# Optimization experiments

Measured on AMD Instinct MI355X. Metric: run time of the kernel, lower is better.

Reference implementation:

```python
import jax, jax.numpy as jnp
import numpy as np

C = 64
CQ = C // 4
G = 8  # group norm groups
EPS_GN = 1e-5
POS_COEF = 0.1


def setup_inputs() -> dict:
    key = jax.random.key(0)
    ks = jax.random.split(key, 12)
    B, N = 2, 4096
    return {
        "context_features": jax.random.normal(ks[0], (B, C, N), jnp.float32),
        "motion_features": jax.random.normal(ks[1], (B, C, N), jnp.float32),
        "xyz1": jax.random.uniform(ks[2], (B, N, 3), jnp.float32),
        # tied q/k conv weight (Conv1d k=1, no bias): (C//4, C)
        "Wqk": jax.random.normal(ks[3], (CQ, C), jnp.float32) * 0.1,
        # v_conv: Conv1d(C, C, 1) with bias
        "Wv": jax.random.normal(ks[4], (C, C), jnp.float32) * 0.1,
        "bv": jax.random.normal(ks[5], (C,), jnp.float32) * 0.1,
        # trans_conv: Conv1d(C, C, 1) with bias
        "Wt": jax.random.normal(ks[6], (C, C), jnp.float32) * 0.1,
        "bt": jax.random.normal(ks[7], (C,), jnp.float32) * 0.1,
        # GroupNorm(8, C) affine params
        "gn_w": jax.random.normal(ks[8], (C,), jnp.float32) * 0.1 + 1.0,
        "gn_b": jax.random.normal(ks[9], (C,), jnp.float32) * 0.1,
        # PReLU single slope, alpha_gma scalar (init 0 in torch; random here for testing)
        "prelu_a": jnp.float32(0.25) + jax.random.normal(ks[10], (), jnp.float32) * 0.01,
        "alpha": jax.random.normal(ks[11], (), jnp.float32) * 0.1,
    }


def _group_norm(x, w, b):
    # x: (B, C, N)
    B, Cc, N = x.shape
    xg = x.reshape(B, G, Cc // G, N)
    mu = xg.mean(axis=(2, 3), keepdims=True)
    var = xg.var(axis=(2, 3), keepdims=True)
    xn = ((xg - mu) * jax.lax.rsqrt(var + EPS_GN)).reshape(B, Cc, N)
    return xn * w[None, :, None] + b[None, :, None]


def reference(context_features, motion_features, xyz1, Wqk, Wv, bv, Wt, bt, gn_w, gn_b, prelu_a, alpha):
    # --- self attention (tied q/k) ---
    q = jnp.einsum("oc,bcn->bon", Wqk, context_features)  # (B, C/4, N)
    corr = jnp.einsum("bom,bon->bmn", q, q)               # (B, N, N)
    attn = jax.nn.softmax(corr, axis=-1)
    attn = attn / (1e-9 + attn.sum(axis=1, keepdims=True))

    # --- position mask via Gram-trick squared distances ---
    sq = jnp.sum(xyz1 * xyz1, axis=-1)                    # (B, N)
    d = sq[:, :, None] + sq[:, None, :] - 2.0 * jnp.einsum("bid,bjd->bij", xyz1, xyz1)
    d = jnp.maximum(d, 0.0)
    pos_am = d / (1e-9 + d.sum(axis=1, keepdims=True))
    mask = pos_am <= POS_COEF

    local = attn * mask
    local = jax.nn.softmax(local, axis=-1)
    local = local / (1e-9 + local.sum(axis=1, keepdims=True))
    attn = attn + local

    # --- GMA fusion ---
    xv = jnp.einsum("oc,bcn->bon", Wv, motion_features) + bv[None, :, None]
    gma = jnp.einsum("bcm,bmn->bcn", xv, attn)
    res = jnp.einsum("oc,bcn->bon", Wt, motion_features - gma) + bt[None, :, None]
    gr = _group_norm(res, gn_w, gn_b)
    gr = jnp.where(gr >= 0, gr, prelu_a * gr)  # PReLU
    return alpha * gr + motion_features
```

## Files before the change

kernel.cpp:

```cpp
#include <hip/hip_runtime.h>
#include <hip/hip_bf16.h>
#include <cstdio>

#define NB 2
#define NN 4096
#define NC 64
#define NQ 16
#define POS_COEF 0.1f

#define OFF_QT   0u
#define OFF_QK   131072u
#define OFF_XYZ4 262144u
#define OFF_XYZK 294912u
#define OFF_IRS1 327680u
#define OFF_IRS2 335872u
#define OFF_THR  344064u
#define OFF_ICS1 352256u
#define OFF_FLAG 360448u
#define OFF_XVB  360464u
#define OFF_SUMS 622608u
#define OFF_GN   622616u
#define OFF_CS2  622648u
#define OFF_GMA  630840u
#define OFF_G2   1155128u
// ... 222 lines not shown
__global__ __launch_bounds__(256) void p1_rs1(
    const float* __restrict__ qt, const float* __restrict__ qk,
    float* __restrict__ irs1) {
  const int tid = threadIdx.x;
  const int b = blockIdx.x >> 8;
  const int m0 = (blockIdx.x & 255) << 4;
  const int w = tid >> 6, lane = tid & 63;
  const float* qb = qt + (size_t)b * NN * 16;
  const float* kb = qk + (size_t)b * 16 * NN;
  const int mA = m0 + w, mB = m0 + w + 4, mC = m0 + w + 8, mD = m0 + w + 12;
  LQROW(ma, qb + (size_t)mA * 16)
  LQROW(mb, qb + (size_t)mB * 16)
  LQROW(mc, qb + (size_t)mC * 16)
  LQROW(md, qb + (size_t)mD * 16)
  float sA = 0.f, sB = 0.f, sC = 0.f, sD = 0.f;
  for (int it = 0; it < 16; ++it) {
    const int n0 = (it << 8) + (lane << 2);
    LKPL(kb, n0)
    sA += __expf(fminf(DOTC(ma0,ma1,ma2,ma3,x), 80.f));
    sA += __expf(fminf(DOTC(ma0,ma1,ma2,ma3,y), 80.f));
    sA += __expf(fminf(DOTC(ma0,ma1,ma2,ma3,z), 80.f));
    sA += __expf(fminf(DOTC(ma0,ma1,ma2,ma3,w), 80.f));
    sB += __expf(fminf(DOTC(mb0,mb1,mb2,mb3,x), 80.f));
    sB += __expf(fminf(DOTC(mb0,mb1,mb2,mb3,y), 80.f));
    sB += __expf(fminf(DOTC(mb0,mb1,mb2,mb3,z), 80.f));
    sB += __expf(fminf(DOTC(mb0,mb1,mb2,mb3,w), 80.f));
    sC += __expf(fminf(DOTC(mc0,mc1,mc2,mc3,x), 80.f));
    sC += __expf(fminf(DOTC(mc0,mc1,mc2,mc3,y), 80.f));
    sC += __expf(fminf(DOTC(mc0,mc1,mc2,mc3,z), 80.f));
    sC += __expf(fminf(DOTC(mc0,mc1,mc2,mc3,w), 80.f));
    sD += __expf(fminf(DOTC(md0,md1,md2,md3,x), 80.f));
    sD += __expf(fminf(DOTC(md0,md1,md2,md3,y), 80.f));
    sD += __expf(fminf(DOTC(md0,md1,md2,md3,z), 80.f));
    sD += __expf(fminf(DOTC(md0,md1,md2,md3,w), 80.f));
  }
  WRED(sA) WRED(sB) WRED(sC) WRED(sD)
  if (lane == 0) {
    irs1[b * NN + mA] = rcpf_(sA);
    irs1[b * NN + mB] = rcpf_(sB);
    irs1[b * NN + mC] = rcpf_(sC);
    irs1[b * NN + mD] = rcpf_(sD);
  }
}

__global__ __launch_bounds__(256) void p3_rs2(
    const float* __restrict__ qt, const float* __restrict__ qk,
    const float* __restrict__ xyz4, const float* __restrict__ xyzk,
    const float* __restrict__ irs1, const float* __restrict__ ics1,
    const float* __restrict__ thr, float* __restrict__ irs2) {
  const int tid = threadIdx.x;
  const int b = blockIdx.x >> 8;
  const int m0 = (blockIdx.x & 255) << 4;
  const int w = tid >> 6, lane = tid & 63;
  const float* qb = qt + (size_t)b * NN * 16;
  const float* kb = qk + (size_t)b * 16 * NN;
  const float* xk = xyzk + (size_t)b * 4 * NN;
  const int mA = m0 + w, mB = m0 + w + 4, mC = m0 + w + 8, mD = m0 + w + 12;
  LQROW(ma, qb + (size_t)mA * 16)
  LQROW(mb, qb + (size_t)mB * 16)
  LQROW(mc, qb + (size_t)mC * 16)
  LQROW(md, qb + (size_t)mD * 16)
  const float4 pmA = *(const float4*)(xyz4 + ((size_t)b * NN + mA) * 4);
  const float4 pmB = *(const float4*)(xyz4 + ((size_t)b * NN + mB) * 4);
  const float4 pmC = *(const float4*)(xyz4 + ((size_t)b * NN + mC) * 4);
  const float4 pmD = *(const float4*)(xyz4 + ((size_t)b * NN + mD) * 4);
  const float rA = irs1[b * NN + mA];
  const float rB = irs1[b * NN + mB];
  const float rC = irs1[b * NN + mC];
  const float rD = irs1[b * NN + mD];
  float sA = 0.f, sB = 0.f, sC = 0.f, sD = 0.f;
#define P3C(S, M0,M1,M2,M3, PM, R, C) { \
    float corr_ = DOTC(M0,M1,M2,M3,C); \
    float a1v_ = __expf(fminf(corr_, 80.f)) * (R) * ic.C; \
    float dd_ = (PM).w + pw.C - 2.f * ((PM).x * px.C + (PM).y * py.C + (PM).z * pz.C); \
    dd_ = fmaxf(dd_, 0.f); \
    float l0_ = (dd_ <= th.C) ? a1v_ : 0.f; \
    S += __expf(l0_); }
  for (int it = 0; it < 16; ++it) {
    const int n0 = (it << 8) + (lane << 2);
    LKPL(kb, n0)
    const float4 px = *(const float4*)(xk + 0*NN + n0);
    const float4 py = *(const float4*)(xk + 1*NN + n0);
    const float4 pz = *(const float4*)(xk + 2*NN + n0);
    const float4 pw = *(const float4*)(xk + 3*NN + n0);
    const float4 ic = *(const float4*)(ics1 + b * NN + n0);
    const float4 th = *(const float4*)(thr + b * NN + n0);
    P3C(sA, ma0,ma1,ma2,ma3, pmA, rA, x)
    P3C(sA, ma0,ma1,ma2,ma3, pmA, rA, y)
    P3C(sA, ma0,ma1,ma2,ma3, pmA, rA, z)
    P3C(sA, ma0,ma1,ma2,ma3, pmA, rA, w)
    P3C(sB, mb0,mb1,mb2,mb3, pmB, rB, x)
    P3C(sB, mb0,mb1,mb2,mb3, pmB, rB, y)
    P3C(sB, mb0,mb1,mb2,mb3, pmB, rB, z)
    P3C(sB, mb0,mb1,mb2,mb3, pmB, rB, w)
    P3C(sC, mc0,mc1,mc2,mc3, pmC, rC, x)
    P3C(sC, mc0,mc1,mc2,mc3, pmC, rC, y)
    P3C(sC, mc0,mc1,mc2,mc3, pmC, rC, z)
    P3C(sC, mc0,mc1,mc2,mc3, pmC, rC, w)
    P3C(sD, md0,md1,md2,md3, pmD, rD, x)
    P3C(sD, md0,md1,md2,md3, pmD, rD, y)
    P3C(sD, md0,md1,md2,md3, pmD, rD, z)
    P3C(sD, md0,md1,md2,md3, pmD, rD, w)
  }
#undef P3C
  WRED(sA) WRED(sB) WRED(sC) WRED(sD)
  if (lane == 0) {
    irs2[b * NN + mA] = rcpf_(sA);
    irs2[b * NN + mB] = rcpf_(sB);
    irs2[b * NN + mC] = rcpf_(sC);
    irs2[b * NN + mD] = rcpf_(sD);
  }
}

__global__ __launch_bounds__(256) void k7_gma(
    const float* __restrict__ qt, const float* __restrict__ xyz4,
    const unsigned short* __restrict__ xvb,
    const float* __restrict__ irs1, const float* __restrict__ irs2,
    const float* __restrict__ ics1, const float* __restrict__ thr,
    float* __restrict__ g1, float* __restrict__ g2, float* __restrict__ cs2) {
  const int tid = threadIdx.x;
  const int bid = blockIdx.x;
  const int msl = bid & 7;
  const int nb = (bid >> 3) & 63;
  const int b = bid >> 9;
  const int n0 = nb << 6;
  const int mstart = msl << 9;
  __shared__ __align__(16) unsigned short attns1[64 * 72];
  __shared__ __align__(16) unsigned short attns2[64 * 72];
  __shared__ __align__(16) unsigned short xvs[64 * 72];
  const float* qb = qt + (size_t)b * NN * 16;
  const float* pb = xyz4 + (size_t)b * NN * 4;
  const int ni = tid & 63, aw = tid >> 6;
  const int na = n0 + ni;
  const float* qnp = qb + (size_t)na * 16;
  LQROW(q, qnp)
  const float4 pn = *(const float4*)(pb + (size_t)na * 4);
  const float ics1n = ics1[b * NN + na];
  const float thr_n = thr[b * NN + na];
  const int lane = tid & 63, wv = tid >> 6;
  const int lr = lane & 15, quad = lane >> 4;
  const int nw = wv << 4;
  f32x4v acc0 = {0,0,0,0}, acc1 = {0,0,0,0}, acc2 = {0,0,0,0}, acc3 = {0,0,0,0};
  f32x4v d0 = {0,0,0,0}, d1 = {0,0,0,0}, d2 = {0,0,0,0}, d3 = {0,0,0,0};
  float csacc = 0.f;
#define COMPA(MOFF, D1, D2) { \
    const int m_ = __builtin_amdgcn_readfirstlane(mw + (MOFF)); \
    const float* qm_ = qb + (size_t)m_ * 16; \
    LQROW(wq, qm_) \
    float corr_ = DOT16M(q0, q1, q2, q3, wq0, wq1, wq2, wq3); \
    const float4 pm_ = *(const float4*)(pb + (size_t)m_ * 4); \
    float a1v_ = __expf(fminf(corr_, 80.f)) * irs1[b * NN + m_] * ics1n; \
    float dd_ = pm_.w + pn.w - 2.f * (pm_.x * pn.x + pm_.y * pn.y + pm_.z * pn.z); \
    dd_ = fmaxf(dd_, 0.f); \
    float l0_ = (dd_ <= thr_n) ? a1v_ : 0.f; \
    float l2n_ = __expf(l0_) * irs2[b * NN + m_]; \
    D1 = f2bf(a1v_); D2 = f2bf(l2n_); csacc += l2n_; }
  for (int mt = 0; mt < 8; ++mt) {
    const int m0 = mstart + (mt << 6);
    __syncthreads();
    {
      const int c = tid >> 2, part = tid & 3;
      const unsigned short* src = xvb + ((size_t)b * 64 + c) * NN + m0 + part * 16;
      unsigned short* dst = xvs + c * 72 + part * 16;
      *(uint4*)dst = *(const uint4*)src;
      *(uint4*)(dst + 8) = *(const uint4*)(src + 8);
    }
    const int mw = m0 + (aw << 4);
#pragma unroll
    for (int g = 0; g < 4; ++g) {
      ushort4 u1, u2;
      COMPA(g * 4 + 0, u1.x, u2.x)
      COMPA(g * 4 + 1, u1.y, u2.y)
      COMPA(g * 4 + 2, u1.z, u2.z)
      COMPA(g * 4 + 3, u1.w, u2.w)
      *(ushort4*)(attns1 + ni * 72 + (aw << 4) + (g << 2)) = u1;
      *(ushort4*)(attns2 + ni * 72 + (aw << 4) + (g << 2)) = u2;
    }
    __syncthreads();
#pragma unroll
    for (int h = 0; h < 2; ++h) {
      const bf16x8 a1 = *(const bf16x8*)(attns1 + (nw + lr) * 72 + h * 32 + quad * 8);
      const bf16x8 a2 = *(const bf16x8*)(attns2 + (nw + lr) * 72 + h * 32 + quad * 8);
      const bf16x8 b0 = *(const bf16x8*)(xvs + (lr) * 72 + h * 32 + quad * 8);
      const bf16x8 b1 = *(const bf16x8*)(xvs + (16 + lr) * 72 + h * 32 + quad * 8);
      const bf16x8 b2 = *(const bf16x8*)(xvs + (32 + lr) * 72 + h * 32 + quad * 8);
      const bf16x8 b3 = *(const bf16x8*)(xvs + (48 + lr) * 72 + h * 32 + quad * 8);
      acc0 = __builtin_amdgcn_mfma_f32_16x16x32_bf16(a1, b0, acc0, 0, 0, 0);
      acc1 = __builtin_amdgcn_mfma_f32_16x16x32_bf16(a1, b1, acc1, 0, 0, 0);
      acc2 = __builtin_amdgcn_mfma_f32_16x16x32_bf16(a1, b2, acc2, 0, 0, 0);
      acc3 = __builtin_amdgcn_mfma_f32_16x16x32_bf16(a1, b3, acc3, 0, 0, 0);
      d0 = __builtin_amdgcn_mfma_f32_16x16x32_bf16(a2, b0, d0, 0, 0, 0);
      d1 = __builtin_amdgcn_mfma_f32_16x16x32_bf16(a2, b1, d1, 0, 0, 0);
      d2 = __builtin_amdgcn_mfma_f32_16x16x32_bf16(a2, b2, d2, 0, 0, 0);
      d3 = __builtin_amdgcn_mfma_f32_16x16x32_bf16(a2, b3, d3, 0, 0, 0);
    }
  }
#undef COMPA
  atomicAdd(&cs2[b * NN + na], csacc);
#define EPI(ACC, DST, CT) { \
    float* g_ = (DST) + ((size_t)b * NN + n0 + nw + (quad << 2)) * 64 + (CT) * 16 + lr; \
    atomicAdd(g_ + 0,   ACC[0]); \
    atomicAdd(g_ + 64,  ACC[1]); \
    atomicAdd(g_ + 128, ACC[2]); \
    atomicAdd(g_ + 192, ACC[3]); }
  EPI(acc0, g1, 0) EPI(acc1, g1, 1) EPI(acc2, g1, 2) EPI(acc3, g1, 3)
  EPI(d0, g2, 0) EPI(d1, g2, 1) EPI(d2, g2, 2) EPI(d3, g2, 3)
#undef EPI
}


__global__ __launch_bounds__(256) void p1m_corr(
    const unsigned short* __restrict__ qbh, const unsigned short* __restrict__ qbl,
    float* __restrict__ rs1raw, unsigned short* __restrict__ a0g) {
  const int tid = threadIdx.x;
  const int nt = blockIdx.x & 63;
  const int mt = (blockIdx.x >> 6) & 63;
  const int b  = blockIdx.x >> 12;
  const int m0 = mt << 6, n0 = nt << 6;
  const int w = tid >> 6, l = tid & 63;
  const int lr = l & 15, quad = l >> 4;
  const int qk8 = (quad & 1) << 3;
  __shared__ __align__(16) unsigned short t0[64 * 72];
  const unsigned short* qh = qbh + (size_t)b * NN * 16;
  const unsigned short* qlo = qbl + (size_t)b * NN * 16;
  const int arow = m0 + (w << 4) + lr;
  const bf16x8 afrag = *(const bf16x8*)((quad < 2 ? qh : qlo) + (size_t)arow * 16 + qk8);
  f32x4v acc0 = {0,0,0,0}, acc1 = {0,0,0,0}, acc2 = {0,0,0,0}, acc3 = {0,0,0,0};
#define DOS(ACC, S) { \
    const int brow_ = n0 + ((S) << 4) + lr; \
    const bf16x8 bhh_ = *(const bf16x8*)(qh + (size_t)brow_ * 16 + qk8); \
    const bf16x8 bll_ = *(const bf16x8*)(qlo + (size_t)brow_ * 16 + qk8); \
    ACC = __builtin_amdgcn_mfma_f32_16x16x32_bf16(afrag, bhh_, ACC, 0, 0, 0); \
    ACC = __builtin_amdgcn_mfma_f32_16x16x32_bf16(afrag, bll_, ACC, 0, 0, 0); }
  DOS(acc0, 0) DOS(acc1, 1) DOS(acc2, 2) DOS(acc3, 3)
#undef DOS
  unsigned short* tw = t0 + (w << 4) * 72;
#define EPW(ACC, S) { \
    tw[((quad << 2) + 0) * 72 + ((S) << 4) + lr] = f2bf(__expf(fminf(ACC[0], 80.f))); \
    tw[((quad << 2) + 1) * 72 + ((S) << 4) + lr] = f2bf(__expf(fminf(ACC[1], 80.f))); \
    tw[((quad << 2) + 2) * 72 + ((S) << 4) + lr] = f2bf(__expf(fminf(ACC[2], 80.f))); \
    tw[((quad << 2) + 3) * 72 + ((S) << 4) + lr] = f2bf(__expf(fminf(ACC[3], 80.f))); }
  EPW(acc0, 0) EPW(acc1, 1) EPW(acc2, 2) EPW(acc3, 3)
#undef EPW
  __syncthreads();
  const int row = tid >> 2, cb = (tid & 3) << 4;
  const unsigned short* src = t0 + row * 72 + cb;
  const uint4 u0 = *(const uint4*)(src);
  const uint4 u1 = *(const uint4*)(src + 8);
  unsigned short* dst = a0g + (size_t)b * NN * NN + (size_t)(m0 + row) * NN + n0 + cb;
  *(uint4*)dst = u0;
  *(uint4*)(dst + 8) = u1;
  float s = 0.f;
#define SUM2(U) { s += bf2f((unsigned short)((U) & 0xffffu)) + bf2f((unsigned short)((U) >> 16)); }
  SUM2(u0.x) SUM2(u0.y) SUM2(u0.z) SUM2(u0.w)
  SUM2(u1.x) SUM2(u1.y) SUM2(u1.z) SUM2(u1.w)
#undef SUM2
  s += __shfl_xor(s, 1);
  s += __shfl_xor(s, 2);
  if ((tid & 3) == 0) atomicAdd(&rs1raw[b * NN + m0 + row], s);
}

__global__ __launch_bounds__(256) void k_inv(
    const float* __restrict__ raw, float* __restrict__ irs1) {
  const int i = blockIdx.x * 256 + threadIdx.x;
  irs1[i] = rcpf_(raw[i]);
}

__global__ __launch_bounds__(256) void p2r_cs1(
    const unsigned short* __restrict__ a0g, const float* __restrict__ irs1,
    float* __restrict__ ics1) {
  const int tid = threadIdx.x;
  const int w = tid >> 6, l = tid & 63;
  const int bi = blockIdx.x;
  const int b = bi >> 10;
  const int n = ((bi & 1023) << 2) + w;
  const unsigned short* row = a0g + ((size_t)b * NN + n) * NN;
  const float* ir = irs1 + b * NN;
  float s = 0.f;
#pragma unroll
  for (int it = 0; it < 8; ++it) {
    const int m = (it << 9) + (l << 3);
    const uint4 u = *(const uint4*)(row + m);
    const float4 i0 = *(const float4*)(ir + m);
    const float4 i1 = *(const float4*)(ir + m + 4);
    s = fmaf(bf2f((unsigned short)(u.x & 0xffffu)), i0.x, s);
    s = fmaf(bf2f((unsigned short)(u.x >> 16)),     i0.y, s);
    s = fmaf(bf2f((unsigned short)(u.y & 0xffffu)), i0.z, s);
    s = fmaf(bf2f((unsigned short)(u.y >> 16)),     i0.w, s);
    s = fmaf(bf2f((unsigned short)(u.z & 0xffffu)), i1.x, s);
    s = fmaf(bf2f((unsigned short)(u.z >> 16)),     i1.y, s);
    s = fmaf(bf2f((unsigned short)(u.w & 0xffffu)), i1.z, s);
    s = fmaf(bf2f((unsigned short)(u.w >> 16)),     i1.w, s);
  }
  WRED(s)
  if (l == 0) ics1[b * NN + n] = rcpf_(1e-9f + s);
}

__global__ __launch_bounds__(256) void p3w_rs2(
    const float* __restrict__ xyz4, const float* __restrict__ xyzk,
    const float* __restrict__ irs1, const float* __restrict__ ics1,
    const float* __restrict__ thr, float* __restrict__ irs2,
    const unsigned short* __restrict__ a0g, unsigned short* __restrict__ aeg) {
  const int tid = threadIdx.x;
  const int b = blockIdx.x >> 9;
  const int m0 = (blockIdx.x & 511) << 3;
  const int w = tid >> 6, lane = tid & 63;
  const float* xk = xyzk + (size_t)b * 4 * NN;
  const unsigned short* ab = a0g + (size_t)b * NN * NN;
  unsigned short* eb = aeg + (size_t)b * NN * NN;
  const int mA = m0 + (w << 1), mB = mA + 1;
  const float4 pmA = *(const float4*)(xyz4 + ((size_t)b * NN + mA) * 4);
  const float4 pmB = *(const float4*)(xyz4 + ((size_t)b * NN + mB) * 4);
  const float rA = irs1[b * NN + mA];
  const float rB = irs1[b * NN + mB];
  float sA = 0.f, sB = 0.f;
#define P3E(S, OUT, A0W, SH, PM, R, PX, PY, PZ, PW, IC, TH) { \
    float a1v_ = bf2f((unsigned short)(((A0W) >> (SH)) & 0xffffu)) * (R) * (IC); \
    float dd_ = (PM).w + (PW) - 2.f * ((PM).x * (PX) + (PM).y * (PY) + (PM).z * (PZ)); \
    dd_ = fmaxf(dd_, 0.f); \
    float l0_ = (dd_ <= (TH)) ? a1v_ : 0.f; \
    const unsigned short us_ = f2bf(__expf(l0_)); OUT = us_; S += bf2f(us_); }
  for (int it = 0; it < 8; ++it) {
    const int n0 = (it << 9) + (lane << 3);
    const float4 pxl = *(const float4*)(xk + 0*NN + n0);
    const float4 pxh = *(const float4*)(xk + 0*NN + n0 + 4);
    const float4 pyl = *(const float4*)(xk + 1*NN + n0);
    const float4 pyh = *(const float4*)(xk + 1*NN + n0 + 4);
    const float4 pzl = *(const float4*)(xk + 2*NN + n0);
    const float4 pzh = *(const float4*)(xk + 2*NN + n0 + 4);
    const float4 pwl = *(const float4*)(xk + 3*NN + n0);
    const float4 pwh = *(const float4*)(xk + 3*NN + n0 + 4);
    const float4 icl = *(const float4*)(ics1 + b * NN + n0);
    const float4 ich = *(const float4*)(ics1 + b * NN + n0 + 4);
    const float4 thl = *(const float4*)(thr + b * NN + n0);
    const float4 thh = *(const float4*)(thr + b * NN + n0 + 4);
    const uint4 rAu = *(const uint4*)(ab + (size_t)mA * NN + n0);
    const uint4 rBu = *(const uint4*)(ab + (size_t)mB * NN + n0);
    unsigned short e0, e1, e2, e3, e4, e5, e6, e7;
    P3E(sA, e0, rAu.x, 0,  pmA, rA, pxl.x, pyl.x, pzl.x, pwl.x, icl.x, thl.x)
    P3E(sA, e1, rAu.x, 16, pmA, rA, pxl.y, pyl.y, pzl.y, pwl.y, icl.y, thl.y)
    P3E(sA, e2, rAu.y, 0,  pmA, rA, pxl.z, pyl.z, pzl.z, pwl.z, icl.z, thl.z)
    P3E(sA, e3, rAu.y, 16, pmA, rA, pxl.w, pyl.w, pzl.w, pwl.w, icl.w, thl.w)
    P3E(sA, e4, rAu.z, 0,  pmA, rA, pxh.x, pyh.x, pzh.x, pwh.x, ich.x, thh.x)
    P3E(sA, e5, rAu.z, 16, pmA, rA, pxh.y, pyh.y, pzh.y, pwh.y, ich.y, thh.y)
    P3E(sA, e6, rAu.w, 0,  pmA, rA, pxh.z, pyh.z, pzh.z, pwh.z, ich.z, thh.z)
    P3E(sA, e7, rAu.w, 16, pmA, rA, pxh.w, pyh.w, pzh.w, pwh.w, ich.w, thh.w)
    {
      uint4 U_;
      U_.x = (unsigned)e0 | ((unsigned)e1 << 16);
      U_.y = (unsigned)e2 | ((unsigned)e3 << 16);
      U_.z = (unsigned)e4 | ((unsigned)e5 << 16);
      U_.w = (unsigned)e6 | ((unsigned)e7 << 16);
      *(uint4*)(eb + (size_t)mA * NN + n0) = U_;
    }
    P3E(sB, e0, rBu.x, 0,  pmB, rB, pxl.x, pyl.x, pzl.x, pwl.x, icl.x, thl.x)
    P3E(sB, e1, rBu.x, 16, pmB, rB, pxl.y, pyl.y, pzl.y, pwl.y, icl.y, thl.y)
    P3E(sB, e2, rBu.y, 0,  pmB, rB, pxl.z, pyl.z, pzl.z, pwl.z, icl.z, thl.z)
    P3E(sB, e3, rBu.y, 16, pmB, rB, pxl.w, pyl.w, pzl.w, pwl.w, icl.w, thl.w)
    P3E(sB, e4, rBu.z, 0,  pmB, rB, pxh.x, pyh.x, pzh.x, pwh.x, ich.x, thh.x)
    P3E(sB, e5, rBu.z, 16, pmB, rB, pxh.y, pyh.y, pzh.y, pwh.y, ich.y, thh.y)
    P3E(sB, e6, rBu.w, 0,  pmB, rB, pxh.z, pyh.z, pzh.z, pwh.z, ich.z, thh.z)
    P3E(sB, e7, rBu.w, 16, pmB, rB, pxh.w, pyh.w, pzh.w, pwh.w, ich.w, thh.w)
    {
      uint4 U_;
      U_.x = (unsigned)e0 | ((unsigned)e1 << 16);
      U_.y = (unsigned)e2 | ((unsigned)e3 << 16);
      U_.z = (unsigned)e4 | ((unsigned)e5 << 16);
      U_.w = (unsigned)e6 | ((unsigned)e7 << 16);
      *(uint4*)(eb + (size_t)mB * NN + n0) = U_;
    }
  }
#undef P3E
  WRED(sA) WRED(sB)
  if (lane == 0) {
    irs2[b * NN + mA] = rcpf_(sA);
    irs2[b * NN + mB] = rcpf_(sB);
  }
}

__global__ __launch_bounds__(256) void p4_cs2(
    const unsigned short* __restrict__ aeg, const float* __restrict__ irs2,
    float* __restrict__ cs2) {
  const int tid = threadIdx.x;
  const int bid = blockIdx.x;
  const int ms = bid & 63;
  const int ng = (bid >> 6) & 7;
  const int b  = bid >> 9;
  const int n2 = (ng << 9) + (tid << 1);
  const unsigned short* eb = aeg + (size_t)b * NN * NN + n2;
  const float* r2 = irs2 + b * NN;
  float s0 = 0.f, s1 = 0.f;
  const int m0 = ms << 6;
#pragma unroll 4
  for (int m = m0; m < m0 + 64; ++m) {
    const unsigned u = *(const unsigned*)(eb + (size_t)m * NN);
    const float r = r2[m];
    s0 += bf2f(f2bf(bf2f((unsigned short)(u & 0xffffu)) * r));
    s1 += bf2f(f2bf(bf2f((unsigned short)(u >> 16)) * r));
  }
  atomicAdd(&cs2[b * NN + n2], s0);
  atomicAdd(&cs2[b * NN + n2 + 1], s1);
}

#define SW(r) ((((r) & 7) << 4) ^ ((((r) >> 3) & 3) << 5))

__global__ __launch_bounds__(256) void k7n_gma(
    const unsigned short* __restrict__ a0g, const unsigned short* __restrict__ aeg,
    const unsigned short* __restrict__ xvb,
    const float* __restrict__ irs1, const float* __restrict__ irs2,
    const float* __restrict__ ics1, const float* __restrict__ cs2,
    float* __restrict__ gma) {
  const int tid = threadIdx.x;
  const int bid = blockIdx.x;
  const int msl = bid & 3;
  const int nb  = (bid >> 2) & 63;
  const int b   = bid >> 8;
  const int n0 = nb << 6;
  const int mstart = msl << 10;
  __shared__ __align__(16) unsigned short attns1[2][64 * 64];
  __shared__ __align__(16) unsigned short attns2[2][64 * 64];
  __shared__ __align__(16) unsigned short xvs[2][64 * 64];
  const unsigned short* ab = a0g + (size_t)b * NN * NN;
  const unsigned short* ebp = aeg + (size_t)b * NN * NN;
  const float* irs1b = irs1 + b * NN;
  const float* irs2b = irs2 + b * NN;
  const int w = tid >> 6, l = tid & 63;
  const int lrow0 = (w << 4) + ((l >> 3) << 1);
  const int nc8 = (l & 7) << 3;
  const int gcol = n0 + nc8;
  const int xc = tid >> 2, xpart = tid & 3;
  const unsigned short* xvp = xvb + ((size_t)b * 64 + xc) * NN;
  const int lr = l & 15, quad = l >> 4;
  const int nw = w << 4;
  f32x4v acc0 = {0,0,0,0}, acc1 = {0,0,0,0}, acc2 = {0,0,0,0}, acc3 = {0,0,0,0};
  f32x4v d0 = {0,0,0,0}, d1 = {0,0,0,0}, d2 = {0,0,0,0}, d3 = {0,0,0,0};

  uint4 pa0A, pa1A, pe0A, pe1A, pv0A, pv1A;
  uint4 pa0B, pa1B, pe0B, pe1B, pv0B, pv1B;
  float r1aA, r1bA, r2aA, r2bA, r1aB, r1bB, r2aB, r2bB;

#define ISSUE(S, MT) { \
    const int m0_ = mstart + ((MT) << 6); \
    const size_t ra_ = (size_t)(m0_ + lrow0) * NN + gcol; \
    pa0##S = *(const uint4*)(ab + ra_); \
    pa1##S = *(const uint4*)(ab + ra_ + NN); \
    pe0##S = *(const uint4*)(ebp + ra_); \
    pe1##S = *(const uint4*)(ebp + ra_ + NN); \
    pv0##S = *(const uint4*)(xvp + m0_ + (xpart << 4)); \
    pv1##S = *(const uint4*)(xvp + m0_ + (xpart << 4) + 8); \
    r1a##S = irs1b[m0_ + lrow0]; r1b##S = irs1b[m0_ + lrow0 + 1]; \
    r2a##S = irs2b[m0_ + lrow0]; r2b##S = irs2b[m0_ + lrow0 + 1]; }

#define CVW(D0, D1, SH, J, R0, R1, ARR) { \
    const float v0_ = bf2f((unsigned short)(((D0) >> (SH)) & 0xffffu)) * (R0); \
    const float v1_ = bf2f((unsigned short)(((D1) >> (SH)) & 0xffffu)) * (R1); \
    const unsigned pk_ = (unsigned)f2bf(v0_) | ((unsigned)f2bf(v1_) << 16); \
    const int nl_ = nc8 + (J); \
    *(unsigned*)((char*)(ARR) + ((((nl_) << 7) + (lrow0 << 1)) ^ SW(nl_))) = pk_; }

#define WR8(U0, U1, R0, R1, ARR) \
    CVW(U0.x, U1.x, 0,  0, R0, R1, ARR) CVW(U0.x, U1.x, 16, 1, R0, R1, ARR) \
    CVW(U0.y, U1.y, 0,  2, R0, R1, ARR) CVW(U0.y, U1.y, 16, 3, R0, R1, ARR) \
    CVW(U0.z, U1.z, 0,  4, R0, R1, ARR) CVW(U0.z, U1.z, 16, 5, R0, R1, ARR) \
    CVW(U0.w, U1.w, 0,  6, R0, R1, ARR) CVW(U0.w, U1.w, 16, 7, R0, R1, ARR)

#define STX(XARR, PV0, PV1) { \
    const int xb_ = (xc << 7) + (xpart << 5); \
    *(uint4*)((char*)(XARR) + ((xb_) ^ SW(xc))) = PV0; \
    *(uint4*)((char*)(XARR) + ((xb_ + 16) ^ SW(xc))) = PV1; }

#define LDSW(ARR, ROW, H, Q) \
    (*(const bf16x8*)((const char*)(ARR) + \
      ((((ROW) << 7) + ((H) << 6) + ((Q) << 4)) ^ SW(ROW))))

#define MPH(A1P, A2P, XVP_) { \
    for (int h = 0; h < 2; ++h) { \
      const bf16x8 fa1 = LDSW(A1P, nw + lr, h, quad); \
      const bf16x8 fa2 = LDSW(A2P, nw + lr, h, quad); \
      const bf16x8 fb0 = LDSW(XVP_, lr, h, quad); \
      const bf16x8 fb1 = LDSW(XVP_, 16 + lr, h, quad); \
      const bf16x8 fb2 = LDSW(XVP_, 32 + lr, h, quad); \
      const bf16x8 fb3 = LDSW(XVP_, 48 + lr, h, quad); \
      acc0 = __builtin_amdgcn_mfma_f32_16x16x32_bf16(fa1, fb0, acc0, 0, 0, 0); \
      acc1 = __builtin_amdgcn_mfma_f32_16x16x32_bf16(fa1, fb1, acc1, 0, 0, 0); \
      acc2 = __builtin_amdgcn_mfma_f32_16x16x32_bf16(fa1, fb2, acc2, 0, 0, 0); \
      acc3 = __builtin_amdgcn_mfma_f32_16x16x32_bf16(fa1, fb3, acc3, 0, 0, 0); \
      d0 = __builtin_amdgcn_mfma_f32_16x16x32_bf16(fa2, fb0, d0, 0, 0, 0); \
      d1 = __builtin_amdgcn_mfma_f32_16x16x32_bf16(fa2, fb1, d1, 0, 0, 0); \
      d2 = __builtin_amdgcn_mfma_f32_16x16x32_bf16(fa2, fb2, d2, 0, 0, 0); \
      d3 = __builtin_amdgcn_mfma_f32_16x16x32_bf16(fa2, fb3, d3, 0, 0, 0); \
    } }

  ISSUE(A, 0)
  ISSUE(B, 1)
  for (int mt = 0; mt < 16; mt += 2) {
    WR8(pa0A, pa1A, r1aA, r1bA, attns1[0])
    WR8(pe0A, pe1A, r2aA, r2bA, attns2[0])
    STX(xvs[0], pv0A, pv1A)
    __syncthreads();
    if (mt + 2 < 16) { ISSUE(A, mt + 2) }
    MPH(attns1[0], attns2[0], xvs[0])
    WR8(pa0B, pa1B, r1aB, r1bB, attns1[1])
    WR8(pe0B, pe1B, r2aB, r2bB, attns2[1])
    STX(xvs[1], pv0B, pv1B)
    __syncthreads();
    if (mt + 3 < 16) { ISSUE(B, mt + 3) }
    MPH(attns1[1], attns2[1], xvs[1])
  }
#undef ISSUE
#undef CVW
#undef WR8
#undef STX
#undef LDSW
#undef MPH
  float w10, w11, w12, w13, w20, w21, w22, w23;
  {
    const int nr = n0 + nw + (quad << 2);
    w10 = ics1[b * NN + nr + 0]; w20 = rcpf_(1e-9f + cs2[b * NN + nr + 0]);
    w11 = ics1[b * NN + nr + 1]; w21 = rcpf_(1e-9f + cs2[b * NN + nr + 1]);
    w12 = ics1[b * NN + nr + 2]; w22 = rcpf_(1e-9f + cs2[b * NN + nr + 2]);
    w13 = ics1[b * NN + nr + 3]; w23 = rcpf_(1e-9f + cs2[b * NN + nr + 3]);
  }
#define EPI(ACC, DD, CT) { \
    float* g_ = gma + ((size_t)b * NN + n0 + nw + (quad << 2)) * 64 + (CT) * 16 + lr; \
    atomicAdd(g_ + 0,   fmaf(ACC[0], w10, DD[0] * w20)); \
    atomicAdd(g_ + 64,  fmaf(ACC[1], w11, DD[1] * w21)); \
    atomicAdd(g_ + 128, fmaf(ACC[2], w12, DD[2] * w22)); \
    atomicAdd(g_ + 192, fmaf(ACC[3], w13, DD[3] * w23)); }
  EPI(acc0, d0, 0) EPI(acc1, d1, 1) EPI(acc2, d2, 2) EPI(acc3, d3, 3)
#undef EPI
}


__global__ __launch_bounds__(256) void p2_cs1(
    const float* __restrict__ qt, const float* __restrict__ qk,
    const float* __restrict__ irs1, float* __restrict__ ics1) {
  const int tid = threadIdx.x;
  const int b = blockIdx.x >> 8;
  const int n0t = (blockIdx.x & 255) << 4;
  const int w = tid >> 6, lane = tid & 63;
  const float* qb = qt + (size_t)b * NN * 16;
  const float* kb = qk + (size_t)b * 16 * NN;
  const int nA = n0t + w, nB = n0t + w + 4, nC = n0t + w + 8, nD = n0t + w + 12;
  LQROW(na, qb + (size_t)nA * 16)
  LQROW(nb, qb + (size_t)nB * 16)
  LQROW(nc, qb + (size_t)nC * 16)
  LQROW(nd, qb + (size_t)nD * 16)
  float sA = 0.f, sB = 0.f, sC = 0.f, sD = 0.f;
  for (int it = 0; it < 16; ++it) {
    const int m0 = (it << 8) + (lane << 2);
    LKPL(kb, m0)
    const float4 r1 = *(const float4*)(irs1 + b * NN + m0);
    sA = fmaf(__expf(fminf(DOTC(na0,na1,na2,na3,x), 80.f)), r1.x, sA);
    sA = fmaf(__expf(fminf(DOTC(na0,na1,na2,na3,y), 80.f)), r1.y, sA);
    sA = fmaf(__expf(fminf(DOTC(na0,na1,na2,na3,z), 80.f)), r1.z, sA);
    sA = fmaf(__expf(fminf(DOTC(na0,na1,na2,na3,w), 80.f)), r1.w, sA);
    sB = fmaf(__expf(fminf(DOTC(nb0,nb1,nb2,nb3,x), 80.f)), r1.x, sB);
    sB = fmaf(__expf(fminf(DOTC(nb0,nb1,nb2,nb3,y), 80.f)), r1.y, sB);
    sB = fmaf(__expf(fminf(DOTC(nb0,nb1,nb2,nb3,z), 80.f)), r1.z, sB);
    sB = fmaf(__expf(fminf(DOTC(nb0,nb1,nb2,nb3,w), 80.f)), r1.w, sB);
    sC = fmaf(__expf(fminf(DOTC(nc0,nc1,nc2,nc3,x), 80.f)), r1.x, sC);
    sC = fmaf(__expf(fminf(DOTC(nc0,nc1,nc2,nc3,y), 80.f)), r1.y, sC);
    sC = fmaf(__expf(fminf(DOTC(nc0,nc1,nc2,nc3,z), 80.f)), r1.z, sC);
    sC = fmaf(__expf(fminf(DOTC(nc0,nc1,nc2,nc3,w), 80.f)), r1.w, sC);
    sD = fmaf(__expf(fminf(DOTC(nd0,nd1,nd2,nd3,x), 80.f)), r1.x, sD);
    sD = fmaf(__expf(fminf(DOTC(nd0,nd1,nd2,nd3,y), 80.f)), r1.y, sD);
    sD = fmaf(__expf(fminf(DOTC(nd0,nd1,nd2,nd3,z), 80.f)), r1.z, sD);
    sD = fmaf(__expf(fminf(DOTC(nd0,nd1,nd2,nd3,w), 80.f)), r1.w, sD);
  }
  WRED(sA) WRED(sB) WRED(sC) WRED(sD)
  if (lane == 0) {
    ics1[b * NN + nA] = rcpf_(1e-9f + sA);
    ics1[b * NN + nB] = rcpf_(1e-9f + sB);
    ics1[b * NN + nC] = rcpf_(1e-9f + sC);
    ics1[b * NN + nD] = rcpf_(1e-9f + sD);
  }
}

__global__ __launch_bounds__(256) void k8_res(
    const void* __restrict__ mot, const void* __restrict__ wt,
    const void* __restrict__ bt, const float* __restrict__ flag,
    float* __restrict__ g1_res, const float* __restrict__ g2,
    const float* __restrict__ cs2, float* __restrict__ gn,
    const float* __restrict__ ics1, int g1mode) {
  const bool f32 = flag[0] > 0.5f;
  const int tid = threadIdx.x;
  const int bid = blockIdx.x;
  const int b = bid >> 9;
  const int n0 = (bid & 511) << 3;
  __shared__ float wtT[64 * 65];
  __shared__ float bts[64];
  __shared__ float md[8 * 64];
  __shared__ float gs[8], gss[8];
  for (int i = tid; i < 4096; i += 256) {
    int o = i & 63, c = i >> 6;
    wtT[c * 65 + o] = ldin(wt, o * 64 + c, f32);
  }
  if (tid < 64) bts[tid] = ldin(bt, tid, f32);
  if (tid < 8) { gs[tid] = 0.f; gss[tid] = 0.f; }
#pragma unroll
  for (int r = 0; r < 2; ++r) {
    const int idx = tid * 2 + r;
    const int c = idx & 63, nl = idx >> 6;
    const size_t gi = ((size_t)b * NN + n0 + nl) * 64 + c;
    float gmav;
    if (g1mode == 2) {
      gmav = g1_res[gi];
    } else {
      const float ics2n = rcpf_(1e-9f + cs2[b * NN + n0 + nl]);
      float g1v = g1_res[gi];
      if (g1mode == 1) g1v *= ics1[b * NN + n0 + nl];
      gmav = fmaf(g2[gi], ics2n, g1v);
    }
    md[nl * 64 + c] = ldin(mot, ((size_t)b * 64 + c) * NN + n0 + nl, f32) - gmav;
  }
  __syncthreads();
  const int o = tid & 63, ng = tid >> 6;
  const int nl0 = ng * 2, nl1 = ng * 2 + 1;
  float a0 = bts[o], a1 = bts[o];
#pragma unroll 8
  for (int c = 0; c < 64; ++c) {
    float w = wtT[c * 65 + o];
    a0 = fmaf(w, md[nl0 * 64 + c], a0);
    a1 = fmaf(w, md[nl1 * 64 + c], a1);
  }
  g1_res[((size_t)b * NN + n0 + nl0) * 64 + o] = a0;
  g1_res[((size_t)b * NN + n0 + nl1) * 64 + o] = a1;
  atomicAdd(&gs[o >> 3], a0 + a1);
  atomicAdd(&gss[o >> 3], a0 * a0 + a1 * a1);
  __syncthreads();
  if (tid < 8) atomicAdd(&gn[b * 8 + tid], gs[tid]);
  else if (tid < 16) atomicAdd(&gn[16 + b * 8 + (tid - 8)], gss[tid - 8]);
}

__global__ __launch_bounds__(256) void k9_out(
    const float* __restrict__ res, const float* __restrict__ gn,
    const void* __restrict__ mot,
    const void* __restrict__ gnw, const void* __restrict__ gnb,
    const void* __restrict__ pa, const void* __restrict__ al,
    const float* __restrict__ flag, void* __restrict__ out) {
  const bool f32 = flag[0] > 0.5f;
  const int idx = blockIdx.x * 256 + threadIdx.x;
  const int n = idx & 4095;
  const int c = (idx >> 12) & 63;
  const int b = idx >> 18;
  const int g = c >> 3;
  const float inv_cnt = 1.f / 32768.f;
  float mean = gn[b * 8 + g] * inv_cnt;
  float var = gn[16 + b * 8 + g] * inv_cnt - mean * mean;
  var = fmaxf(var, 0.f);
  float rstd = rsqrtf(var + 1e-5f);
  float r = res[((size_t)b * NN + n) * 64 + c];
  float y = (r - mean) * rstd * ldin(gnw, c, f32) + ldin(gnb, c, f32);
  float slope = ldin(pa, 0, f32);
  y = (y >= 0.f) ? y : slope * y;
  float o = ldin(al, 0, f32) * y + ldin(mot, idx, f32);
  if (f32) ((float*)out)[idx] = o;
  else     ((__hip_bfloat16*)out)[idx] = __float2bfloat16(o);
}

extern "C" void kernel_launch(void* const* d_in, const int* in_sizes, int n_in,
                              void* d_out, int out_size, void* d_ws, size_t ws_size,
                              hipStream_t stream) {
  const void* ctx = d_in[0];
  const void* mot = d_in[1];
  const void* xyz = d_in[2];
  const void* wqk = d_in[3];
  const void* wv  = d_in[4];
  const void* bv  = d_in[5];
  const void* wt  = d_in[6];
  const void* bt  = d_in[7];
  const void* gnw = d_in[8];
  const void* gnb = d_in[9];
  const void* pa  = d_in[10];
  const void* al  = d_in[11];
  float* ws = (float*)d_ws;
  const bool big = ws_size >= (size_t)FULL_F * sizeof(float);

  if (ws_size < (size_t)WS_TOTAL * sizeof(float))
    fprintf(stderr, "[gma3d] WARNING ws_size=%zu < needed %zu\n",
            ws_size, (size_t)WS_TOTAL * sizeof(float));

  hipMemsetAsync(ws + OFF_SUMS, 0, (size_t)ZERO_F * sizeof(float), stream);

  k0_detect<<<1, 256, 0, stream>>>((const unsigned short*)ctx, ws + OFF_FLAG);
  k1_q_xyz<<<32, 256, 0, stream>>>(ctx, xyz, wqk, ws + OFF_FLAG,
                                   ws + OFF_QT, ws + OFF_QK,
                                   ws + OFF_XYZ4, ws + OFF_XYZK, ws + OFF_SUMS,
                                   big ? (unsigned short*)(ws + OFF_QBH) : (unsigned short*)nullptr,
                                   big ? (unsigned short*)(ws + OFF_QBL) : (unsigned short*)nullptr);
  k2_xv<<<128, 256, 0, stream>>>(mot, wv, bv, ws + OFF_FLAG,
                                 (unsigned short*)(ws + OFF_XVB));
  k2b_thr<<<32, 256, 0, stream>>>(ws + OFF_XYZ4, ws + OFF_SUMS, ws + OFF_THR);

  if (big) {
    unsigned short* a0 = (unsigned short*)(ws + OFF_A0);
    unsigned short* ae = (unsigned short*)(ws + OFF_AE);
    p1m_corr<<<8192, 256, 0, stream>>>((const unsigned short*)(ws + OFF_QBH),
                                       (const unsigned short*)(ws + OFF_QBL),
                                       ws + OFF_RS1R, a0);
    k_inv<<<32, 256, 0, stream>>>(ws + OFF_RS1R, ws + OFF_IRS1);
    p2r_cs1<<<2048, 256, 0, stream>>>(a0, ws + OFF_IRS1, ws + OFF_ICS1);
    p3w_rs2<<<1024, 256, 0, stream>>>(ws + OFF_XYZ4, ws + OFF_XYZK,
                                      ws + OFF_IRS1, ws + OFF_ICS1, ws + OFF_THR,
                                      ws + OFF_IRS2, a0, ae);
    p4_cs2<<<1024, 256, 0, stream>>>(ae, ws + OFF_IRS2, ws + OFF_CS2);
    k7n_gma<<<512, 256, 0, stream>>>(a0, ae,
                                     (const unsigned short*)(ws + OFF_XVB),
                                     ws + OFF_IRS1, ws + OFF_IRS2,
                                     ws + OFF_ICS1, ws + OFF_CS2,
                                     ws + OFF_GMA);
    k8_res<<<1024, 256, 0, stream>>>(mot, wt, bt, ws + OFF_FLAG,
                                     ws + OFF_GMA, ws + OFF_G2, ws + OFF_CS2,
                                     ws + OFF_GN, ws + OFF_ICS1, 2);
  } else {
    p1_rs1<<<512, 256, 0, stream>>>(ws + OFF_QT, ws + OFF_QK, ws + OFF_IRS1);
    p2_cs1<<<512, 256, 0, stream>>>(ws + OFF_QT, ws + OFF_QK, ws + OFF_IRS1, ws + OFF_ICS1);
    p3_rs2<<<512, 256, 0, stream>>>(ws + OFF_QT, ws + OFF_QK,
                                    ws + OFF_XYZ4, ws + OFF_XYZK,
                                    ws + OFF_IRS1, ws + OFF_ICS1, ws + OFF_THR,
                                    ws + OFF_IRS2);
    k7_gma<<<1024, 256, 0, stream>>>(ws + OFF_QT, ws + OFF_XYZ4,
                                     (const unsigned short*)(ws + OFF_XVB),
                                     ws + OFF_IRS1, ws + OFF_IRS2,
                                     ws + OFF_ICS1, ws + OFF_THR,
                                     ws + OFF_GMA, ws + OFF_G2, ws + OFF_CS2);
    k8_res<<<1024, 256, 0, stream>>>(mot, wt, bt, ws + OFF_FLAG,
                                     ws + OFF_GMA, ws + OFF_G2, ws + OFF_CS2,
                                     ws + OFF_GN, ws + OFF_ICS1, 0);
  }

  k9_out<<<2048, 256, 0, stream>>>(ws + OFF_GMA, ws + OFF_GN, mot, gnw, gnb, pa, al,
                                   ws + OFF_FLAG, d_out);
}
```

Before: 269.1 us.

## Process four rows per wave in rs2, raise MFMA priority, transpose output via LDS

The position-mask/exp kernel now handles four attention rows per wave instead of two. This reuses the loaded xyz, threshold and column-scale vectors across more rows and halves the grid. The GMA matmul phase raises wave priority around its MFMA block with s_setprio. The final GroupNorm/PReLU/residual kernel is rewritten to read the (N,C) result tile with float4 loads, transpose it through shared memory, and write (C,N) output in coalesced order instead of using strided gathers. The rs2 change adds register pressure and halves the number of blocks, which may reduce occupancy.

```diff
diff --git a/kernel.cpp b/kernel.cpp
--- a/kernel.cpp
+++ b/kernel.cpp
@@ -548,24 +548,44 @@
     const float* __restrict__ thr, float* __restrict__ irs2,
     const unsigned short* __restrict__ a0g, unsigned short* __restrict__ aeg) {
   const int tid = threadIdx.x;
-  const int b = blockIdx.x >> 9;
-  const int m0 = (blockIdx.x & 511) << 3;
+  const int b = blockIdx.x >> 8;
+  const int m0 = (blockIdx.x & 255) << 4;
   const int w = tid >> 6, lane = tid & 63;
   const float* xk = xyzk + (size_t)b * 4 * NN;
   const unsigned short* ab = a0g + (size_t)b * NN * NN;
   unsigned short* eb = aeg + (size_t)b * NN * NN;
-  const int mA = m0 + (w << 1), mB = mA + 1;
+  const int mA = m0 + (w << 2), mB = mA + 1, mC = mA + 2, mD = mA + 3;
   const float4 pmA = *(const float4*)(xyz4 + ((size_t)b * NN + mA) * 4);
   const float4 pmB = *(const float4*)(xyz4 + ((size_t)b * NN + mB) * 4);
+  const float4 pmC = *(const float4*)(xyz4 + ((size_t)b * NN + mC) * 4);
+  const float4 pmD = *(const float4*)(xyz4 + ((size_t)b * NN + mD) * 4);
   const float rA = irs1[b * NN + mA];
   const float rB = irs1[b * NN + mB];
-  float sA = 0.f, sB = 0.f;
+  const float rC = irs1[b * NN + mC];
+  const float rD = irs1[b * NN + mD];
+  float sA = 0.f, sB = 0.f, sC = 0.f, sD = 0.f;
 #define P3E(S, OUT, A0W, SH, PM, R, PX, PY, PZ, PW, IC, TH) { \
     float a1v_ = bf2f((unsigned short)(((A0W) >> (SH)) & 0xffffu)) * (R) * (IC); \
     float dd_ = (PM).w + (PW) - 2.f * ((PM).x * (PX) + (PM).y * (PY) + (PM).z * (PZ)); \
     dd_ = fmaxf(dd_, 0.f); \
     float l0_ = (dd_ <= (TH)) ? a1v_ : 0.f; \
     const unsigned short us_ = f2bf(__expf(l0_)); OUT = us_; S += bf2f(us_); }
+#define PROW(S, RU, PM, R, MROW) { \
+    unsigned short e0, e1, e2, e3, e4, e5, e6, e7; \
+    P3E(S, e0, RU.x, 0,  PM, R, pxl.x, pyl.x, pzl.x, pwl.x, icl.x, thl.x) \
+    P3E(S, e1, RU.x, 16, PM, R, pxl.y, pyl.y, pzl.y, pwl.y, icl.y, thl.y) \
+    P3E(S, e2, RU.y, 0,  PM, R, pxl.z, pyl.z, pzl.z, pwl.z, icl.z, thl.z) \
+    P3E(S, e3, RU.y, 16, PM, R, pxl.w, pyl.w, pzl.w, pwl.w, icl.w, thl.w) \
+    P3E(S, e4, RU.z, 0,  PM, R, pxh.x, pyh.x, pzh.x, pwh.x, ich.x, thh.x) \
+    P3E(S, e5, RU.z, 16, PM, R, pxh.y, pyh.y, pzh.y, pwh.y, ich.y, thh.y) \
+    P3E(S, e6, RU.w, 0,  PM, R, pxh.z, pyh.z, pzh.z, pwh.z, ich.z, thh.z) \
+    P3E(S, e7, RU.w, 16, PM, R, pxh.w, pyh.w, pzh.w, pwh.w, ich.w, thh.w) \
+    uint4 U_; \
+    U_.x = (unsigned)e0 | ((unsigned)e1 << 16); \
+    U_.y = (unsigned)e2 | ((unsigned)e3 << 16); \
+    U_.z = (unsigned)e4 | ((unsigned)e5 << 16); \
+    U_.w = (unsigned)e6 | ((unsigned)e7 << 16); \
+    *(uint4*)(eb + (size_t)(MROW) * NN + n0) = U_; }
   for (int it = 0; it < 8; ++it) {
     const int n0 = (it << 9) + (lane << 3);
     const float4 pxl = *(const float4*)(xk + 0*NN + n0);
@@ -582,45 +602,21 @@
     const float4 thh = *(const float4*)(thr + b * NN + n0 + 4);
     const uint4 rAu = *(const uint4*)(ab + (size_t)mA * NN + n0);
     const uint4 rBu = *(const uint4*)(ab + (size_t)mB * NN + n0);
-    unsigned short e0, e1, e2, e3, e4, e5, e6, e7;
-    P3E(sA, e0, rAu.x, 0,  pmA, rA, pxl.x, pyl.x, pzl.x, pwl.x, icl.x, thl.x)
-    P3E(sA, e1, rAu.x, 16, pmA, rA, pxl.y, pyl.y, pzl.y, pwl.y, icl.y, thl.y)
-    P3E(sA, e2, rAu.y, 0,  pmA, rA, pxl.z, pyl.z, pzl.z, pwl.z, icl.z, thl.z)
-    P3E(sA, e3, rAu.y, 16, pmA, rA, pxl.w, pyl.w, pzl.w, pwl.w, icl.w, thl.w)
-    P3E(sA, e4, rAu.z, 0,  pmA, rA, pxh.x, pyh.x, pzh.x, pwh.x, ich.x, thh.x)
-    P3E(sA, e5, rAu.z, 16, pmA, rA, pxh.y, pyh.y, pzh.y, pwh.y, ich.y, thh.y)
-    P3E(sA, e6, rAu.w, 0,  pmA, rA, pxh.z, pyh.z, pzh.z, pwh.z, ich.z, thh.z)
-    P3E(sA, e7, rAu.w, 16, pmA, rA, pxh.w, pyh.w, pzh.w, pwh.w, ich.w, thh.w)
-    {
-      uint4 U_;
-      U_.x = (unsigned)e0 | ((unsigned)e1 << 16);
-      U_.y = (unsigned)e2 | ((unsigned)e3 << 16);
-      U_.z = (unsigned)e4 | ((unsigned)e5 << 16);
-      U_.w = (unsigned)e6 | ((unsigned)e7 << 16);
-      *(uint4*)(eb + (size_t)mA * NN + n0) = U_;
-    }
-    P3E(sB, e0, rBu.x, 0,  pmB, rB, pxl.x, pyl.x, pzl.x, pwl.x, icl.x, thl.x)
-    P3E(sB, e1, rBu.x, 16, pmB, rB, pxl.y, pyl.y, pzl.y, pwl.y, icl.y, thl.y)
-    P3E(sB, e2, rBu.y, 0,  pmB, rB, pxl.z, pyl.z, pzl.z, pwl.z, icl.z, thl.z)
-    P3E(sB, e3, rBu.y, 16, pmB, rB, pxl.w, pyl.w, pzl.w, pwl.w, icl.w, thl.w)
-    P3E(sB, e4, rBu.z, 0,  pmB, rB, pxh.x, pyh.x, pzh.x, pwh.x, ich.x, thh.x)
-    P3E(sB, e5, rBu.z, 16, pmB, rB, pxh.y, pyh.y, pzh.y, pwh.y, ich.y, thh.y)
-    P3E(sB, e6, rBu.w, 0,  pmB, rB, pxh.z, pyh.z, pzh.z, pwh.z, ich.z, thh.z)
-    P3E(sB, e7, rBu.w, 16, pmB, rB, pxh.w, pyh.w, pzh.w, pwh.w, ich.w, thh.w)
-    {
-      uint4 U_;
-      U_.x = (unsigned)e0 | ((unsigned)e1 << 16);
-      U_.y = (unsigned)e2 | ((unsigned)e3 << 16);
-      U_.z = (unsigned)e4 | ((unsigned)e5 << 16);
-      U_.w = (unsigned)e6 | ((unsigned)e7 << 16);
-      *(uint4*)(eb + (size_t)mB * NN + n0) = U_;
-    }
-  }
+    const uint4 rCu = *(const uint4*)(ab + (size_t)mC * NN + n0);
+    const uint4 rDu = *(const uint4*)(ab + (size_t)mD * NN + n0);
+    PROW(sA, rAu, pmA, rA, mA)
+    PROW(sB, rBu, pmB, rB, mB)
+    PROW(sC, rCu, pmC, rC, mC)
+    PROW(sD, rDu, pmD, rD, mD)
+  }
+#undef PROW
 #undef P3E
-  WRED(sA) WRED(sB)
+  WRED(sA) WRED(sB) WRED(sC) WRED(sD)
   if (lane == 0) {
     irs2[b * NN + mA] = rcpf_(sA);
     irs2[b * NN + mB] = rcpf_(sB);
+    irs2[b * NN + mC] = rcpf_(sC);
+    irs2[b * NN + mD] = rcpf_(sD);
   }
 }
 
@@ -720,6 +716,7 @@
       ((((ROW) << 7) + ((H) << 6) + ((Q) << 4)) ^ SW(ROW))))
 
 #define MPH(A1P, A2P, XVP_) { \
+    __builtin_amdgcn_s_setprio(1); \
     for (int h = 0; h < 2; ++h) { \
       const bf16x8 fa1 = LDSW(A1P, nw + lr, h, quad); \
       const bf16x8 fa2 = LDSW(A2P, nw + lr, h, quad); \
@@ -735,7 +732,8 @@
       d1 = __builtin_amdgcn_mfma_f32_16x16x32_bf16(fa2, fb1, d1, 0, 0, 0); \
       d2 = __builtin_amdgcn_mfma_f32_16x16x32_bf16(fa2, fb2, d2, 0, 0, 0); \
       d3 = __builtin_amdgcn_mfma_f32_16x16x32_bf16(fa2, fb3, d3, 0, 0, 0); \
-    } }
+    } \
+    __builtin_amdgcn_s_setprio(0); }
 
   ISSUE(A, 0)
   ISSUE(B, 1)
@@ -879,30 +877,58 @@
   else if (tid < 16) atomicAdd(&gn[16 + b * 8 + (tid - 8)], gss[tid - 8]);
 }
 
-__global__ __launch_bounds__(256) void k9_out(
+__global__ __launch_bounds__(256) void k9t_out(
     const float* __restrict__ res, const float* __restrict__ gn,
     const void* __restrict__ mot,
     const void* __restrict__ gnw, const void* __restrict__ gnb,
     const void* __restrict__ pa, const void* __restrict__ al,
     const float* __restrict__ flag, void* __restrict__ out) {
   const bool f32 = flag[0] > 0.5f;
-  const int idx = blockIdx.x * 256 + threadIdx.x;
-  const int n = idx & 4095;
-  const int c = (idx >> 12) & 63;
-  const int b = idx >> 18;
-  const int g = c >> 3;
+  const int tid = threadIdx.x;
+  const int b = blockIdx.x >> 7;
+  const int n0 = (blockIdx.x & 127) << 5;
+  __shared__ float ty[64][33];
   const float inv_cnt = 1.f / 32768.f;
-  float mean = gn[b * 8 + g] * inv_cnt;
-  float var = gn[16 + b * 8 + g] * inv_cnt - mean * mean;
-  var = fmaxf(var, 0.f);
-  float rstd = rsqrtf(var + 1e-5f);
-  float r = res[((size_t)b * NN + n) * 64 + c];
-  float y = (r - mean) * rstd * ldin(gnw, c, f32) + ldin(gnb, c, f32);
-  float slope = ldin(pa, 0, f32);
-  y = (y >= 0.f) ? y : slope * y;
-  float o = ldin(al, 0, f32) * y + ldin(mot, idx, f32);
-  if (f32) ((float*)out)[idx] = o;
-  else     ((__hip_bfloat16*)out)[idx] = __float2bfloat16(o);
+  const float slope = ldin(pa, 0, f32);
+  const float alv = ldin(al, 0, f32);
+  {
+    const int row = tid >> 3;
+    const int cseg = (tid & 7) << 3;
+    const int g = cseg >> 3;
+    const float mean = gn[b * 8 + g] * inv_cnt;
+    float var = gn[16 + b * 8 + g] * inv_cnt - mean * mean;
+    var = fmaxf(var, 0.f);
+    const float rstd = rsqrtf(var + 1e-5f);
+    const float* rp = res + ((size_t)b * NN + n0 + row) * 64 + cseg;
+    const float4 v0 = *(const float4*)rp;
+    const float4 v1 = *(const float4*)(rp + 4);
+#define GNP(V, J) { \
+      const int c_ = cseg + (J); \
+      float y_ = (V - mean) * rstd * ldin(gnw, c_, f32) + ldin(gnb, c_, f32); \
+      y_ = (y_ >= 0.f) ? y_ : slope * y_; \
+      ty[c_][row] = alv * y_; }
+    GNP(v0.x, 0) GNP(v0.y, 1) GNP(v0.z, 2) GNP(v0.w, 3)
+    GNP(v1.x, 4) GNP(v1.y, 5) GNP(v1.z, 6) GNP(v1.w, 7)
+#undef GNP
+  }
+  __syncthreads();
+  {
+    const int c = tid >> 2;
+    const int ns = (tid & 3) << 3;
+    const size_t mbase = ((size_t)b * 64 + c) * NN + n0 + ns;
+    if (f32) {
+      const float* mp = (const float*)mot + mbase;
+      float* op = (float*)out + mbase;
+#pragma unroll
+      for (int j = 0; j < 8; ++j) op[j] = ty[c][ns + j] + mp[j];
+    } else {
+      const __hip_bfloat16* mp = (const __hip_bfloat16*)mot + mbase;
+      __hip_bfloat16* op = (__hip_bfloat16*)out + mbase;
+#pragma unroll
+      for (int j = 0; j < 8; ++j)
+        op[j] = __float2bfloat16(ty[c][ns + j] + __bfloat162float(mp[j]));
+    }
+  }
 }
 
 extern "C" void kernel_launch(void* const* d_in, const int* in_sizes, int n_in,
@@ -947,9 +973,9 @@
                                        ws + OFF_RS1R, a0);
     k_inv<<<32, 256, 0, stream>>>(ws + OFF_RS1R, ws + OFF_IRS1);
     p2r_cs1<<<2048, 256, 0, stream>>>(a0, ws + OFF_IRS1, ws + OFF_ICS1);
-    p3w_rs2<<<1024, 256, 0, stream>>>(ws + OFF_XYZ4, ws + OFF_XYZK,
-                                      ws + OFF_IRS1, ws + OFF_ICS1, ws + OFF_THR,
-                                      ws + OFF_IRS2, a0, ae);
+    p3w_rs2<<<512, 256, 0, stream>>>(ws + OFF_XYZ4, ws + OFF_XYZK,
+                                     ws + OFF_IRS1, ws + OFF_ICS1, ws + OFF_THR,
+                                     ws + OFF_IRS2, a0, ae);
     p4_cs2<<<1024, 256, 0, stream>>>(ae, ws + OFF_IRS2, ws + OFF_CS2);
     k7n_gma<<<512, 256, 0, stream>>>(a0, ae,
                                      (const unsigned short*)(ws + OFF_XVB),
@@ -976,6 +1002,6 @@
                                      ws + OFF_GN, ws + OFF_ICS1, 0);
   }
 
-  k9_out<<<2048, 256, 0, stream>>>(ws + OFF_GMA, ws + OFF_GN, mot, gnw, gnb, pa, al,
+  k9t_out<<<256, 256, 0, stream>>>(ws + OFF_GMA, ws + OFF_GN, mot, gnw, gnb, pa, al,
                                    ws + OFF_FLAG, d_out);
 }
```

Measured after the change: 264.6 us. About the same (-1.6%).
